# Kernel tuning notes

Hardware: AMD Instinct MI355X
Metric: run time of the kernel (lower is better)

Reference implementation:

```python
import jax, jax.numpy as jnp
import numpy as np

B, S, DM = 2, 2048, 1024
H, KH, HD = 16, 4, 64  # query heads, kv heads, head_dim
N_REP = H // KH


def rotate_half(u):
    d = u.shape[-1] // 2
    return jnp.concatenate([-u[..., d:], u[..., :d]], axis=-1)


def setup_inputs() -> dict:
    key = jax.random.key(0)
    ks = jax.random.split(key, 7)
    x = jax.random.normal(ks[0], (B, S, DM), dtype=jnp.float32)
    # RoPE tables (real rotary angles for realism)
    inv_freq = 1.0 / (10000.0 ** (jnp.arange(0, HD, 2, dtype=jnp.float32) / HD))
    t = jnp.arange(S, dtype=jnp.float32)
    freqs = jnp.outer(t, inv_freq)                      # [S, HD/2]
    emb = jnp.concatenate([freqs, freqs], axis=-1)      # [S, HD]
    cos, sin = jnp.cos(emb), jnp.sin(emb)
    sc = 0.02
    wq = jax.random.normal(ks[1], (DM, H * HD), dtype=jnp.float32) * sc
    wk = jax.random.normal(ks[2], (DM, KH * HD), dtype=jnp.float32) * sc
    wv = jax.random.normal(ks[3], (DM, KH * HD), dtype=jnp.float32) * sc
    wo = jax.random.normal(ks[4], (H * HD, DM), dtype=jnp.float32) * sc
    return {"x": x, "cos": cos, "sin": sin, "wq": wq, "wk": wk, "wv": wv, "wo": wo}


def reference(x, cos, sin, wq, wk, wv, wo):
    b, s, _ = x.shape
    # QKV projections (no bias)
    q = (x @ wq).reshape(b, s, H, HD)   # [b,s,H,HD]
    k = (x @ wk).reshape(b, s, KH, HD)  # [b,s,KH,HD]
    v = (x @ wv).reshape(b, s, KH, HD)
    # RoPE, broadcast cos/sin over the head axis
    c = cos[None, :s, None, :]
    sn = sin[None, :s, None, :]
    q = q * c + rotate_half(q) * sn
    k = k * c + rotate_half(k) * sn
    # GQA: repeat kv heads (repeat_interleave along head axis)
    k = jnp.repeat(k, N_REP, axis=2)  # [b,s,H,HD]
    v = jnp.repeat(v, N_REP, axis=2)
    # causal attention, full score matrix (non-flash path)
    scores = jnp.einsum("bqhd,bkhd->bhqk", q, k) / jnp.sqrt(jnp.float32(HD))
    causal = jnp.tril(jnp.ones((s, s), dtype=bool))
    scores = jnp.where(causal[None, None], scores, jnp.float32(-jnp.inf))
    attn = jax.nn.softmax(scores, axis=-1)
    out = jnp.einsum("bhqk,bkhd->bqhd", attn, v).reshape(b, s, H * HD)
    return out @ wo
```

## Files before the change

### kernel.cpp

```cpp
#include <hip/hip_runtime.h>
#include <hip/hip_bf16.h>

#define BATCH 2
#define SLEN  2048
#define DM    1024
#define NH    16
#define NKH   4
#define HD    64
#define NCH   4
#define PSTRIDE (BATCH * SLEN * NH * HD)
#define LSTRIDE (BATCH * SLEN * NH)

typedef __attribute__((ext_vector_type(8))) short short8;
typedef __attribute__((ext_vector_type(4))) float f32x4;

static __device__ __forceinline__ short f2bf(float x) {
    unsigned u = __float_as_uint(x);
    u += 0x7fffu + ((u >> 16) & 1u);
    return (short)(u >> 16);
}

static __device__ __forceinline__ void ldg_lds16(const short* g, short* l) {
    __builtin_amdgcn_global_load_lds(
        (const __attribute__((address_space(1))) unsigned int*)(const void*)g,
        (__attribute__((address_space(3))) unsigned int*)(void*)l,
        16, 0, 0);
}

#define QSCALE 0.1803368801f

__global__ __launch_bounds__(256) void prep_all(
    const float* __restrict__ wq, const float* __restrict__ wk,
    const float* __restrict__ wv, const float* __restrict__ wo,
    short* __restrict__ T,
    const float* __restrict__ X, short* __restrict__ Xb)
{
    const int by = blockIdx.y;
    const int t  = threadIdx.x;

    if (by >= 40) {
        const int blk = (by - 40) * 16 + blockIdx.x;
#pragma unroll
        for (int j = 0; j < 16; ++j) {
            const int i = blk * 4096 + j * 256 + t;
            const float4 v0 = ((const float4*)X)[i * 2];
            const float4 v1 = ((const float4*)X)[i * 2 + 1];
            __align__(16) short o[8];
            o[0] = f2bf(v0.x); o[1] = f2bf(v0.y); o[2] = f2bf(v0.z); o[3] = f2bf(v0.w);
            o[4] = f2bf(v1.x); o[5] = f2bf(v1.y); o[6] = f2bf(v1.z); o[7] = f2bf(v1.w);
            ((int4*)Xb)[i] = *(const int4*)o;
        }
        return;
    }

    const float* W; int Nc, rowoff, ntile;
    if (by < 16)      { W = wq; Nc = 1024; rowoff = 0;    ntile = by; }
    else if (by < 20) { W = wk; Nc = 256;  rowoff = 1024; ntile = by - 16; }
    else if (by < 24) { W = wv; Nc = 256;  rowoff = 1280; ntile = by - 20; }
    else              { W = wo; Nc = 1024; rowoff = 1536; ntile = by - 24; }
    const int kt = blockIdx.x * 64;
    const int nt = ntile * 64;
    __shared__ float tile[64][65];

#pragma unroll
    for (int i = 0; i < 4; ++i) {
        const int r = (t >> 4) + i * 16;
        const int c = (t & 15) * 4;
        const float4 v = *(const float4*)(W + (size_t)(kt + r) * Nc + nt + c);
        tile[r][c + 0] = v.x; tile[r][c + 1] = v.y;
        tile[r][c + 2] = v.z; tile[r][c + 3] = v.w;
    }
    __syncthreads();
#pragma unroll
    for (int i = 0; i < 2; ++i) {
        const int rr = (t >> 3) + i * 32;
        const int cc = (t & 7) * 8;
        __align__(16) short o[8];
#pragma unroll
        for (int j = 0; j < 8; ++j) o[j] = f2bf(tile[cc + j][rr]);
        *(int4*)(T + (size_t)(rowoff + nt + rr) * 1024 + kt + cc) = *(const int4*)o;
    }
}

template<int MODE>
__global__ __launch_bounds__(256) void gemm_abt(
    const short* __restrict__ A, const short* __restrict__ Bt,
    int M, int N, int K,
    float* __restrict__ Cf,
    short* __restrict__ Qb, short* __restrict__ Kb, short* __restrict__ Vb,
    const float* __restrict__ cosp, const float* __restrict__ sinp)
{
    const int t    = threadIdx.x;
    const int lane = t & 63;
    const int w    = t >> 6;
    const int l15  = lane & 15;
    const int l4   = lane >> 4;
    const int n0   = blockIdx.x * 128;
    const int m0   = blockIdx.y * 64;
    const int wm   = (w & 1) * 32;
    const int wn   = (w >> 1) * 64;

    __shared__ __align__(16) short As[64 * 64];
    __shared__ __align__(16) short Bs[128 * 64];

    f32x4 acc[2][4];
#pragma unroll
    for (int i = 0; i < 2; ++i)
#pragma unroll
        for (int j = 0; j < 4; ++j) acc[i][j] = (f32x4){0.f, 0.f, 0.f, 0.f};

    for (int kt = 0; kt < K; kt += 64) {
        __syncthreads();
#pragma unroll
        for (int i = 0; i < 2; ++i) {
            const int chunk = i * 256 + t;
            const int r = chunk >> 3;
            const int c = (chunk & 7) * 8;
            ldg_lds16(A + (size_t)(m0 + r) * K + kt + c, &As[chunk * 8]);
        }
#pragma unroll
        for (int i = 0; i < 4; ++i) {
            const int chunk = i * 256 + t;
            const int r = chunk >> 3;
            const int c = (chunk & 7) * 8;
            ldg_lds16(Bt + (size_t)(n0 + r) * K + kt + c, &Bs[chunk * 8]);
        }
        __syncthreads();

#pragma unroll
        for (int k2 = 0; k2 < 2; ++k2) {
            short8 af[2], bf[4];
#pragma unroll
            for (int i = 0; i < 2; ++i)
                af[i] = *(const short8*)&As[(wm + i * 16 + l15) * 64 + k2 * 32 + l4 * 8];
#pragma unroll
            for (int j = 0; j < 4; ++j)
                bf[j] = *(const short8*)&Bs[(wn + j * 16 + l15) * 64 + k2 * 32 + l4 * 8];
#pragma unroll
            for (int i = 0; i < 2; ++i)
#pragma unroll
                for (int j = 0; j < 4; ++j)
                    acc[i][j] = __builtin_amdgcn_mfma_f32_16x16x32_bf16(af[i], bf[j], acc[i][j], 0, 0, 0);
        }
    }

    if (MODE == 1) {
#pragma unroll
        for (int i = 0; i < 2; ++i)
#pragma unroll
            for (int j = 0; j < 4; ++j)
#pragma unroll
                for (int r = 0; r < 4; ++r) {
                    const int m = m0 + wm + i * 16 + l4 * 4 + r;
                    const int n = n0 + wn + j * 16 + l15;
                    Cf[(size_t)m * N + n] = acc[i][j][r];
                }
        return;
    }

    const int colbase = n0 + wn;
    if (colbase < 1024) {
        const int h = colbase >> 6;
#pragma unroll
        for (int i = 0; i < 2; ++i)
#pragma unroll
            for (int r = 0; r < 4; ++r) {
                const int m = m0 + wm + i * 16 + l4 * 4 + r;
                const int b = m >> 11, s = m & (SLEN - 1);
                short* dst = Qb + (((size_t)(b * SLEN + s) * NH + h) << 6);
#pragma unroll
                for (int j = 0; j < 2; ++j) {
                    const int d = j * 16 + l15;
                    const float cv = cosp[s * HD + d];
                    const float sv = sinp[s * HD + d];
                    const float a0 = acc[i][j][r];
                    const float a1 = acc[i][j + 2][r];
                    dst[d]      = f2bf((a0 * cv - a1 * sv) * QSCALE);
                    dst[d + 32] = f2bf((a1 * cv + a0 * sv) * QSCALE);
                }
            }
    } else if (colbase < 1280) {
        const int kh = (colbase - 1024) >> 6;
#pragma unroll
        for (int i = 0; i < 2; ++i)
#pragma unroll
            for (int r = 0; r < 4; ++r) {
                const int m = m0 + wm + i * 16 + l4 * 4 + r;
                const int b = m >> 11, s = m & (SLEN - 1);
                short* dst = Kb + (((size_t)(b * SLEN + s) * NKH + kh) << 6);
#pragma unroll
                for (int j = 0; j < 2; ++j) {
                    const int d = j * 16 + l15;
                    const float cv = cosp[s * HD + d];
                    const float sv = sinp[s * HD + d];
                    const float a0 = acc[i][j][r];
                    const float a1 = acc[i][j + 2][r];
                    dst[d]      = f2bf(a0 * cv - a1 * sv);
                    dst[d + 32] = f2bf(a1 * cv + a0 * sv);
                }
            }
    } else {
        const int kh = (colbase - 1280) >> 6;
#pragma unroll
        for (int i = 0; i < 2; ++i)
#pragma unroll
            for (int r = 0; r < 4; ++r) {
                const int m = m0 + wm + i * 16 + l4 * 4 + r;
                const int b = m >> 11, s = m & (SLEN - 1);
                short* dst = Vb + (((size_t)(b * SLEN + s) * NKH + kh) << 6);
#pragma unroll
                for (int j = 0; j < 4; ++j)
                    dst[j * 16 + l15] = f2bf(acc[i][j][r]);
            }
    }
}

__global__ __launch_bounds__(256) void vtrans_b(
    const short* __restrict__ Vb, short* __restrict__ Vt)
{
    const int s0 = blockIdx.x * 64;
    const int kh = blockIdx.y;
    const int b  = blockIdx.z;
    const int t  = threadIdx.x;
    __shared__ short tile[64][72];

#pragma unroll
    for (int i = 0; i < 2; ++i) {
        const int chunk = i * 256 + t;
        const int r = chunk >> 3;
        const int c = (chunk & 7) * 8;
        *(int4*)&tile[r][c] =
            *(const int4*)(Vb + (((size_t)(b * SLEN + s0 + r) * NKH + kh) << 6) + c);
    }
    __syncthreads();
#pragma unroll
    for (int i = 0; i < 2; ++i) {
        const int chunk = i * 256 + t;
        const int d  = chunk >> 3;
        const int sc = (chunk & 7) * 8;
        __align__(16) short o[8];
#pragma unroll
        for (int j = 0; j < 8; ++j) {
            const int sp = sc + j;
            const int u  = ((sp & 3) << 4) | (sp >> 2);
            o[j] = tile[u][d];
        }
        *(int4*)(Vt + ((size_t)((b * NKH + kh) * HD + d)) * SLEN + s0 + sc) = *(const int4*)o;
    }
}

__global__ __launch_bounds__(256, 4) void flash_mfma(
    const short* __restrict__ Qb,
    const short* __restrict__ Kb,
    const short* __restrict__ Vt,
    short* __restrict__ O,
    float* __restrict__ Op,
    float* __restrict__ Lp)
{
    const int qs = 63 - blockIdx.x;
    const int kc = blockIdx.y & 3;
    if (kc * 16 > qs) return;
    const int kh = blockIdx.y >> 2;
    const int b  = blockIdx.z;
    const int t    = threadIdx.x;
    const int lane = t & 63;
    const int w    = t >> 6;
    const int h    = kh * 4 + w;
    const int l15  = lane & 15;
    const int l4   = lane >> 4;
    const int q0   = qs * 32;
    const int sw   = l15 & 7;

    __shared__ __align__(16) short Ks[2][64 * 64];
    __shared__ __align__(16) short Vs[2][64 * 64];
    __shared__ __align__(16) short Ps[4][16 * 64];

    const int r_st  = t >> 3;
    const int c8_st = t & 7;

    short8 aq[2][2];
#pragma unroll
    for (int i = 0; i < 2; ++i)
#pragma unroll
        for (int ks = 0; ks < 2; ++ks)
            aq[i][ks] = *(const short8*)(
                Qb + ((size_t)((b * SLEN + q0 + i * 16 + l15) * NH + h)) * HD + ks * 32 + l4 * 8);

    f32x4 acc[2][4];
    f32x4 accl[2];
#pragma unroll
    for (int i = 0; i < 2; ++i) {
#pragma unroll
        for (int nt = 0; nt < 4; ++nt) acc[i][nt] = (f32x4){0.f, 0.f, 0.f, 0.f};
        accl[i] = (f32x4){0.f, 0.f, 0.f, 0.f};
    }

    const short8 ones8 = {0x3f80, 0x3f80, 0x3f80, 0x3f80, 0x3f80, 0x3f80, 0x3f80, 0x3f80};

    const int ntiles = (q0 >> 6) + 1;
    const int kt0  = kc * 8;
    const int kend = (kt0 + 8 < ntiles) ? kt0 + 8 : ntiles;

#define STAGE(BI, K0)                                                          \
    {                                                                          \
        _Pragma("unroll")                                                      \
        for (int i_ = 0; i_ < 2; ++i_) {                                       \
            const int r  = i_ * 32 + r_st;                                     \
            const int cs = (c8_st ^ (r & 7)) * 8;                              \
            const int ch = i_ * 256 + t;                                       \
            ldg_lds16(Kb + ((size_t)((b * SLEN + (K0) + r) * NKH + kh)) * HD + cs, \
                      &Ks[BI][ch * 8]);                                        \
            ldg_lds16(Vt + ((size_t)((b * NKH + kh) * HD + r)) * SLEN + (K0) + cs, \
                      &Vs[BI][ch * 8]);                                        \
        }                                                                      \
    }

    STAGE(0, kt0 * 64)

    for (int kt = kt0; kt < kend; ++kt) {
        const int bi = (kt - kt0) & 1;
        __syncthreads();
        if (kt + 1 < kend) STAGE(bi ^ 1, (kt + 1) * 64)

        f32x4 sf[2][4];
#pragma unroll
        for (int i = 0; i < 2; ++i)
#pragma unroll
            for (int f = 0; f < 4; ++f) sf[i][f] = (f32x4){0.f, 0.f, 0.f, 0.f};
#pragma unroll
        for (int ks = 0; ks < 2; ++ks)
#pragma unroll
            for (int f = 0; f < 4; ++f) {
                const short8 bk = *(const short8*)
                    &Ks[bi][(f * 16 + l15) * 64 + ((ks * 4 + l4) ^ sw) * 8];
#pragma unroll
                for (int i = 0; i < 2; ++i)
                    sf[i][f] = __builtin_amdgcn_mfma_f32_16x16x32_bf16(aq[i][ks], bk, sf[i][f], 0, 0, 0);
            }

        if (kt == ntiles - 1) {
            const int k0 = kt * 64;
#pragma unroll
            for (int i = 0; i < 2; ++i)
#pragma unroll
                for (int f = 0; f < 4; ++f)
#pragma unroll
                    for (int r = 0; r < 4; ++r)
                        if (k0 + f * 16 + l15 > q0 + i * 16 + l4 * 4 + r)
                            sf[i][f][r] = -1e30f;
        }

#pragma unroll
        for (int i = 0; i < 2; ++i) {
#pragma unroll
            for (int r = 0; r < 4; ++r) {
                __align__(8) short pk[4];
#pragma unroll
                for (int f = 0; f < 4; ++f) pk[f] = f2bf(exp2f(sf[i][f][r]));
                const int row = l4 * 4 + r;
                *(int2*)&Ps[w][row * 64 + (((l15 >> 1) ^ (row & 7)) << 3) + ((l15 & 1) << 2)] =
                    *(const int2*)pk;
            }
#pragma unroll
            for (int ks = 0; ks < 2; ++ks) {
                const short8 ap = *(const short8*)
                    &Ps[w][l15 * 64 + (((ks * 4 + l4) ^ (l15 & 7)) << 3)];
#pragma unroll
                for (int nt = 0; nt < 4; ++nt) {
                    const short8 bv = *(const short8*)
                        &Vs[bi][(nt * 16 + l15) * 64 + ((ks * 4 + l4) ^ sw) * 8];
                    acc[i][nt] = __builtin_amdgcn_mfma_f32_16x16x32_bf16(ap, bv, acc[i][nt], 0, 0, 0);
                }
                accl[i] = __builtin_amdgcn_mfma_f32_16x16x32_bf16(ap, ones8, accl[i], 0, 0, 0);
            }
        }
    }

    if (q0 < 512) {
#pragma unroll
        for (int i = 0; i < 2; ++i) {
            float rl[4];
#pragma unroll
            for (int r = 0; r < 4; ++r) rl[r] = 1.f / accl[i][r];
#pragma unroll
            for (int nt = 0; nt < 4; ++nt)
#pragma unroll
                for (int r = 0; r < 4; ++r) {
                    const int q = q0 + i * 16 + l4 * 4 + r;
                    O[((size_t)((b * SLEN + q) * NH + h)) * HD + nt * 16 + l15] =
                        f2bf(acc[i][nt][r] * rl[r]);
                }
        }
    } else {
        const size_t pbase = (size_t)kc * PSTRIDE;
#pragma unroll
        for (int i = 0; i < 2; ++i)
#pragma unroll
            for (int nt = 0; nt < 4; ++nt)
#pragma unroll
                for (int r = 0; r < 4; ++r) {
                    const int q = q0 + i * 16 + l4 * 4 + r;
                    Op[pbase + ((size_t)((b * SLEN + q) * NH + h)) * HD + nt * 16 + l15] =
                        acc[i][nt][r];
                }
        if (l15 == 0) {
#pragma unroll
            for (int i = 0; i < 2; ++i)
#pragma unroll
                for (int r = 0; r < 4; ++r) {
                    const int q = q0 + i * 16 + l4 * 4 + r;
                    Lp[(size_t)kc * LSTRIDE + (size_t)(b * SLEN + q) * NH + h] = accl[i][r];
                }
        }
    }
}

__global__ void combine_k(const float* __restrict__ Op, const float* __restrict__ Lp,
                          short* __restrict__ O)
{
    const int idx = blockIdx.x * 256 + threadIdx.x;
    const int dq = idx & 15;
    const int h  = (idx >> 4) & 15;
    const int rr = idx >> 8;
    const int b  = rr / 1536;
    const int s  = 512 + (rr - b * 1536);
    const int nact = (s >> 9) + 1;
    const size_t row = (size_t)(b * SLEN + s) * NH + h;

    float4 o = {0.f, 0.f, 0.f, 0.f};
    float l = 0.f;
    for (int kc = 0; kc < nact; ++kc) {
        const float4 p = *(const float4*)(Op + (size_t)kc * PSTRIDE + row * HD + dq * 4);
        o.x += p.x; o.y += p.y; o.z += p.z; o.w += p.w;
        l += Lp[(size_t)kc * LSTRIDE + row];
    }
    const float rl = 1.f / l;
    __align__(8) short pk[4];
    pk[0] = f2bf(o.x * rl); pk[1] = f2bf(o.y * rl);
    pk[2] = f2bf(o.z * rl); pk[3] = f2bf(o.w * rl);
    *(int2*)(O + row * HD + dq * 4) = *(const int2*)pk;
}

extern "C" void kernel_launch(void* const* d_in, const int* in_sizes, int n_in,
                              void* d_out, int out_size, void* d_ws, size_t ws_size,
                              hipStream_t stream) {
    const float* x    = (const float*)d_in[0];
    const float* cosp = (const float*)d_in[1];
    const float* sinp = (const float*)d_in[2];
    const float* wq   = (const float*)d_in[3];
    const float* wk   = (const float*)d_in[4];
    const float* wv   = (const float*)d_in[5];
    const float* wo   = (const float*)d_in[6];
    float* out = (float*)d_out;

    const int Mrows = BATCH * SLEN;

    short* xb = (short*)d_ws;
    short* Ob = xb;
    short* wT = xb + (size_t)Mrows * 1024;
    short* Qb = wT + (size_t)2560 * 1024;
    short* Kb = Qb + (size_t)Mrows * 1024;
    short* Vt = Kb + (size_t)Mrows * 256;
    short* Vb = Vt + (size_t)Mrows * 256;
    float* Op = (float*)(Vb + (size_t)Mrows * 256);
    float* Lp = Op + (size_t)NCH * PSTRIDE;

    prep_all<<<dim3(16, 48), 256, 0, stream>>>(wq, wk, wv, wo, wT, x, xb);

    gemm_abt<0><<<dim3(1536 / 128, Mrows / 64), 256, 0, stream>>>(
        xb, wT, Mrows, 1536, DM, nullptr, Qb, Kb, Vb, cosp, sinp);

    vtrans_b<<<dim3(SLEN / 64, NKH, BATCH), 256, 0, stream>>>(Vb, Vt);

    flash_mfma<<<dim3(SLEN / 32, NKH * NCH, BATCH), 256, 0, stream>>>(
        Qb, Kb, Vt, Ob, Op, Lp);

    combine_k<<<(BATCH * 1536 * NH * 16) / 256, 256, 0, stream>>>(Op, Lp, Ob);

    gemm_abt<1><<<dim3(DM / 128, Mrows / 64), 256, 0, stream>>>(
        Ob, wT + (size_t)1536 * 1024, Mrows, DM, DM, out,
        nullptr, nullptr, nullptr, nullptr, nullptr);
}
```

Before: 191.1 us.

## Register-prefetch double-buffered pipelines in GEMM and flash attention loops

The GEMM loop is converted from a single LDS buffer with two barriers per k-tile into a double-buffered scheme. The next tile is loaded into registers during compute and written to the alternate LDS buffer afterward, with an XOR swizzle added on the A/B tiles to reduce bank conflicts. The attention kernel replaces its async global-to-LDS staging with the same register prefetch. This aims to overlap global latency with MFMA work and remove one barrier per iteration, at the cost of extra VGPRs and doubled LDS in the GEMM, and __launch_bounds__(256,3) is added to keep occupancy.

```diff
diff --git a/kernel.cpp b/kernel.cpp
--- a/kernel.cpp
+++ b/kernel.cpp
@@ -83,7 +83,7 @@
 }
 
 template<int MODE>
-__global__ __launch_bounds__(256) void gemm_abt(
+__global__ __launch_bounds__(256, 3) void gemm_abt(
     const short* __restrict__ A, const short* __restrict__ Bt,
     int M, int N, int K,
     float* __restrict__ Cf,
@@ -100,8 +100,52 @@
     const int wm   = (w & 1) * 32;
     const int wn   = (w >> 1) * 64;
 
-    __shared__ __align__(16) short As[64 * 64];
-    __shared__ __align__(16) short Bs[128 * 64];
+    __shared__ __align__(16) short As[2][64 * 64];
+    __shared__ __align__(16) short Bs[2][128 * 64];
+
+    int4 areg[2], breg[4];
+
+#define G_GLL(BI, KT)                                                          \
+    {                                                                          \
+        _Pragma("unroll")                                                      \
+        for (int i_ = 0; i_ < 2; ++i_) {                                       \
+            const int ch = i_ * 256 + t;                                       \
+            const int r = ch >> 3, cs = ((ch & 7) ^ (r & 7)) * 8;              \
+            ldg_lds16(A + (size_t)(m0 + r) * K + (KT) + cs, &As[BI][ch * 8]);  \
+        }                                                                      \
+        _Pragma("unroll")                                                      \
+        for (int i_ = 0; i_ < 4; ++i_) {                                       \
+            const int ch = i_ * 256 + t;                                       \
+            const int r = ch >> 3, cs = ((ch & 7) ^ (r & 7)) * 8;              \
+            ldg_lds16(Bt + (size_t)(n0 + r) * K + (KT) + cs, &Bs[BI][ch * 8]); \
+        }                                                                      \
+    }
+
+#define G_LOADREG(KT)                                                          \
+    {                                                                          \
+        _Pragma("unroll")                                                      \
+        for (int i_ = 0; i_ < 2; ++i_) {                                       \
+            const int ch = i_ * 256 + t;                                       \
+            const int r = ch >> 3, cs = ((ch & 7) ^ (r & 7)) * 8;              \
+            areg[i_] = *(const int4*)(A + (size_t)(m0 + r) * K + (KT) + cs);   \
+        }                                                                      \
+        _Pragma("unroll")                                                      \
+        for (int i_ = 0; i_ < 4; ++i_) {                                       \
+            const int ch = i_ * 256 + t;                                       \
+            const int r = ch >> 3, cs = ((ch & 7) ^ (r & 7)) * 8;              \
+            breg[i_] = *(const int4*)(Bt + (size_t)(n0 + r) * K + (KT) + cs);  \
+        }                                                                      \
+    }
+
+#define G_WRITEREG(BI)                                                         \
+    {                                                                          \
+        _Pragma("unroll")                                                      \
+        for (int i_ = 0; i_ < 2; ++i_)                                         \
+            *(int4*)&As[BI][(i_ * 256 + t) * 8] = areg[i_];                    \
+        _Pragma("unroll")                                                      \
+        for (int i_ = 0; i_ < 4; ++i_)                                         \
+            *(int4*)&Bs[BI][(i_ * 256 + t) * 8] = breg[i_];                    \
+    }
 
     f32x4 acc[2][4];
 #pragma unroll
@@ -109,38 +153,33 @@
 #pragma unroll
         for (int j = 0; j < 4; ++j) acc[i][j] = (f32x4){0.f, 0.f, 0.f, 0.f};
 
+    G_GLL(0, 0)
+    G_LOADREG(64)
+
     for (int kt = 0; kt < K; kt += 64) {
+        const int bi = (kt >> 6) & 1;
         __syncthreads();
-#pragma unroll
-        for (int i = 0; i < 2; ++i) {
-            const int chunk = i * 256 + t;
-            const int r = chunk >> 3;
-            const int c = (chunk & 7) * 8;
-            ldg_lds16(A + (size_t)(m0 + r) * K + kt + c, &As[chunk * 8]);
-        }
-#pragma unroll
-        for (int i = 0; i < 4; ++i) {
-            const int chunk = i * 256 + t;
-            const int r = chunk >> 3;
-            const int c = (chunk & 7) * 8;
-            ldg_lds16(Bt + (size_t)(n0 + r) * K + kt + c, &Bs[chunk * 8]);
-        }
-        __syncthreads();
 
 #pragma unroll
         for (int k2 = 0; k2 < 2; ++k2) {
-            short8 af[2], bf[4];
+            const int pc = (((k2 * 4 + l4) ^ (l15 & 7)) << 3);
+            short8 af[2], bfr[4];
 #pragma unroll
             for (int i = 0; i < 2; ++i)
-                af[i] = *(const short8*)&As[(wm + i * 16 + l15) * 64 + k2 * 32 + l4 * 8];
+                af[i] = *(const short8*)&As[bi][(wm + i * 16 + l15) * 64 + pc];
 #pragma unroll
             for (int j = 0; j < 4; ++j)
-                bf[j] = *(const short8*)&Bs[(wn + j * 16 + l15) * 64 + k2 * 32 + l4 * 8];
+                bfr[j] = *(const short8*)&Bs[bi][(wn + j * 16 + l15) * 64 + pc];
 #pragma unroll
             for (int i = 0; i < 2; ++i)
 #pragma unroll
                 for (int j = 0; j < 4; ++j)
-                    acc[i][j] = __builtin_amdgcn_mfma_f32_16x16x32_bf16(af[i], bf[j], acc[i][j], 0, 0, 0);
+                    acc[i][j] = __builtin_amdgcn_mfma_f32_16x16x32_bf16(af[i], bfr[j], acc[i][j], 0, 0, 0);
+        }
+
+        if (kt + 64 < K) {
+            G_WRITEREG(bi ^ 1)
+            if (kt + 128 < K) G_LOADREG(kt + 128)
         }
     }
 
@@ -213,6 +252,9 @@
                     dst[j * 16 + l15] = f2bf(acc[i][j][r]);
             }
     }
+#undef G_GLL
+#undef G_LOADREG
+#undef G_WRITEREG
 }
 
 __global__ __launch_bounds__(256) void vtrans_b(
@@ -278,30 +320,9 @@
     const int r_st  = t >> 3;
     const int c8_st = t & 7;
 
-    short8 aq[2][2];
-#pragma unroll
-    for (int i = 0; i < 2; ++i)
-#pragma unroll
-        for (int ks = 0; ks < 2; ++ks)
-            aq[i][ks] = *(const short8*)(
-                Qb + ((size_t)((b * SLEN + q0 + i * 16 + l15) * NH + h)) * HD + ks * 32 + l4 * 8);
-
-    f32x4 acc[2][4];
-    f32x4 accl[2];
-#pragma unroll
-    for (int i = 0; i < 2; ++i) {
-#pragma unroll
-        for (int nt = 0; nt < 4; ++nt) acc[i][nt] = (f32x4){0.f, 0.f, 0.f, 0.f};
-        accl[i] = (f32x4){0.f, 0.f, 0.f, 0.f};
-    }
-
-    const short8 ones8 = {0x3f80, 0x3f80, 0x3f80, 0x3f80, 0x3f80, 0x3f80, 0x3f80, 0x3f80};
-
-    const int ntiles = (q0 >> 6) + 1;
-    const int kt0  = kc * 8;
-    const int kend = (kt0 + 8 < ntiles) ? kt0 + 8 : ntiles;
-
-#define STAGE(BI, K0)                                                          \
+    int4 kreg[2], vreg[2];
+
+#define F_GLL(BI, K0)                                                          \
     {                                                                          \
         _Pragma("unroll")                                                      \
         for (int i_ = 0; i_ < 2; ++i_) {                                       \
@@ -315,12 +336,56 @@
         }                                                                      \
     }
 
-    STAGE(0, kt0 * 64)
+#define F_LOADREG(K0)                                                          \
+    {                                                                          \
+        _Pragma("unroll")                                                      \
+        for (int i_ = 0; i_ < 2; ++i_) {                                       \
+            const int r  = i_ * 32 + r_st;                                     \
+            const int cs = (c8_st ^ (r & 7)) * 8;                              \
+            kreg[i_] = *(const int4*)(Kb + ((size_t)((b * SLEN + (K0) + r) * NKH + kh)) * HD + cs); \
+            vreg[i_] = *(const int4*)(Vt + ((size_t)((b * NKH + kh) * HD + r)) * SLEN + (K0) + cs); \
+        }                                                                      \
+    }
+
+#define F_WRITEREG(BI)                                                         \
+    {                                                                          \
+        _Pragma("unroll")                                                      \
+        for (int i_ = 0; i_ < 2; ++i_) {                                       \
+            const int ch = i_ * 256 + t;                                       \
+            *(int4*)&Ks[BI][ch * 8] = kreg[i_];                                \
+            *(int4*)&Vs[BI][ch * 8] = vreg[i_];                                \
+        }                                                                      \
+    }
+
+    short8 aq[2][2];
+#pragma unroll
+    for (int i = 0; i < 2; ++i)
+#pragma unroll
+        for (int ks = 0; ks < 2; ++ks)
+            aq[i][ks] = *(const short8*)(
+                Qb + ((size_t)((b * SLEN + q0 + i * 16 + l15) * NH + h)) * HD + ks * 32 + l4 * 8);
+
+    f32x4 acc[2][4];
+    f32x4 accl[2];
+#pragma unroll
+    for (int i = 0; i < 2; ++i) {
+#pragma unroll
+        for (int nt = 0; nt < 4; ++nt) acc[i][nt] = (f32x4){0.f, 0.f, 0.f, 0.f};
+        accl[i] = (f32x4){0.f, 0.f, 0.f, 0.f};
+    }
+
+    const short8 ones8 = {0x3f80, 0x3f80, 0x3f80, 0x3f80, 0x3f80, 0x3f80, 0x3f80, 0x3f80};
+
+    const int ntiles = (q0 >> 6) + 1;
+    const int kt0  = kc * 8;
+    const int kend = (kt0 + 8 < ntiles) ? kt0 + 8 : ntiles;
+
+    F_GLL(0, kt0 * 64)
+    if (kt0 + 1 < kend) F_LOADREG((kt0 + 1) * 64)
 
     for (int kt = kt0; kt < kend; ++kt) {
         const int bi = (kt - kt0) & 1;
         __syncthreads();
-        if (kt + 1 < kend) STAGE(bi ^ 1, (kt + 1) * 64)
 
         f32x4 sf[2][4];
 #pragma unroll
@@ -374,6 +439,11 @@
                 accl[i] = __builtin_amdgcn_mfma_f32_16x16x32_bf16(ap, ones8, accl[i], 0, 0, 0);
             }
         }
+
+        if (kt + 1 < kend) {
+            F_WRITEREG(bi ^ 1)
+            if (kt + 2 < kend) F_LOADREG((kt + 2) * 64)
+        }
     }
 
     if (q0 < 512) {
@@ -413,6 +483,9 @@
                 }
         }
     }
+#undef F_GLL
+#undef F_LOADREG
+#undef F_WRITEREG
 }
 
 __global__ void combine_k(const float* __restrict__ Op, const float* __restrict__ Lp,
```

Result: slower. 297.2 us (+55.5%).

## Swizzle GEMM LDS tiles and process KV in 128-key pairs without double buffering

Applied to the files above, without the earlier changes.

The GEMM kernel now applies an XOR swizzle to its A and B LDS tiles, both when staging and when reading fragments, to avoid LDS bank conflicts. The attention kernel drops its two-tile double-buffered K/V staging. It now loads 128 keys (a pair of 64-key tiles) per sync round into single larger buffers, halving the number of barriers. The cost is that global loads no longer overlap compute. Pairs that run past the causal end rely on the widened mask (kt >= ntiles-1) to zero out the extra tile, which still does the work of loading and computing that extra tile.

```diff
diff --git a/kernel.cpp b/kernel.cpp
--- a/kernel.cpp
+++ b/kernel.cpp
@@ -113,34 +113,33 @@
         __syncthreads();
 #pragma unroll
         for (int i = 0; i < 2; ++i) {
-            const int chunk = i * 256 + t;
-            const int r = chunk >> 3;
-            const int c = (chunk & 7) * 8;
-            ldg_lds16(A + (size_t)(m0 + r) * K + kt + c, &As[chunk * 8]);
+            const int ch = i * 256 + t;
+            const int r = ch >> 3, cs = ((ch & 7) ^ (r & 7)) * 8;
+            ldg_lds16(A + (size_t)(m0 + r) * K + kt + cs, &As[ch * 8]);
         }
 #pragma unroll
         for (int i = 0; i < 4; ++i) {
-            const int chunk = i * 256 + t;
-            const int r = chunk >> 3;
-            const int c = (chunk & 7) * 8;
-            ldg_lds16(Bt + (size_t)(n0 + r) * K + kt + c, &Bs[chunk * 8]);
+            const int ch = i * 256 + t;
+            const int r = ch >> 3, cs = ((ch & 7) ^ (r & 7)) * 8;
+            ldg_lds16(Bt + (size_t)(n0 + r) * K + kt + cs, &Bs[ch * 8]);
         }
         __syncthreads();
 
 #pragma unroll
         for (int k2 = 0; k2 < 2; ++k2) {
-            short8 af[2], bf[4];
+            const int pc = (((k2 * 4 + l4) ^ (l15 & 7)) << 3);
+            short8 af[2], bfr[4];
 #pragma unroll
             for (int i = 0; i < 2; ++i)
-                af[i] = *(const short8*)&As[(wm + i * 16 + l15) * 64 + k2 * 32 + l4 * 8];
+                af[i] = *(const short8*)&As[(wm + i * 16 + l15) * 64 + pc];
 #pragma unroll
             for (int j = 0; j < 4; ++j)
-                bf[j] = *(const short8*)&Bs[(wn + j * 16 + l15) * 64 + k2 * 32 + l4 * 8];
+                bfr[j] = *(const short8*)&Bs[(wn + j * 16 + l15) * 64 + pc];
 #pragma unroll
             for (int i = 0; i < 2; ++i)
 #pragma unroll
                 for (int j = 0; j < 4; ++j)
-                    acc[i][j] = __builtin_amdgcn_mfma_f32_16x16x32_bf16(af[i], bf[j], acc[i][j], 0, 0, 0);
+                    acc[i][j] = __builtin_amdgcn_mfma_f32_16x16x32_bf16(af[i], bfr[j], acc[i][j], 0, 0, 0);
         }
     }
 
@@ -271,12 +270,9 @@
     const int q0   = qs * 32;
     const int sw   = l15 & 7;
 
-    __shared__ __align__(16) short Ks[2][64 * 64];
-    __shared__ __align__(16) short Vs[2][64 * 64];
+    __shared__ __align__(16) short Ks[128 * 64];
+    __shared__ __align__(16) short Vs[64 * 128];
     __shared__ __align__(16) short Ps[4][16 * 64];
-
-    const int r_st  = t >> 3;
-    const int c8_st = t & 7;
 
     short8 aq[2][2];
 #pragma unroll
@@ -298,80 +294,85 @@
     const short8 ones8 = {0x3f80, 0x3f80, 0x3f80, 0x3f80, 0x3f80, 0x3f80, 0x3f80, 0x3f80};
 
     const int ntiles = (q0 >> 6) + 1;
-    const int kt0  = kc * 8;
-    const int kend = (kt0 + 8 < ntiles) ? kt0 + 8 : ntiles;
-
-#define STAGE(BI, K0)                                                          \
-    {                                                                          \
-        _Pragma("unroll")                                                      \
-        for (int i_ = 0; i_ < 2; ++i_) {                                       \
-            const int r  = i_ * 32 + r_st;                                     \
-            const int cs = (c8_st ^ (r & 7)) * 8;                              \
-            const int ch = i_ * 256 + t;                                       \
-            ldg_lds16(Kb + ((size_t)((b * SLEN + (K0) + r) * NKH + kh)) * HD + cs, \
-                      &Ks[BI][ch * 8]);                                        \
-            ldg_lds16(Vt + ((size_t)((b * NKH + kh) * HD + r)) * SLEN + (K0) + cs, \
-                      &Vs[BI][ch * 8]);                                        \
-        }                                                                      \
-    }
-
-    STAGE(0, kt0 * 64)
-
-    for (int kt = kt0; kt < kend; ++kt) {
-        const int bi = (kt - kt0) & 1;
+    const int kt0    = kc * 8;
+    const int kend   = (kt0 + 8 < ntiles) ? kt0 + 8 : ntiles;
+    const int npairs = (kend - kt0 + 1) >> 1;
+
+    for (int p = 0; p < npairs; ++p) {
+        const int tbase = kt0 + 2 * p;
+        const int k0p   = tbase * 64;
         __syncthreads();
-        if (kt + 1 < kend) STAGE(bi ^ 1, (kt + 1) * 64)
-
-        f32x4 sf[2][4];
-#pragma unroll
-        for (int i = 0; i < 2; ++i)
-#pragma unroll
-            for (int f = 0; f < 4; ++f) sf[i][f] = (f32x4){0.f, 0.f, 0.f, 0.f};
-#pragma unroll
-        for (int ks = 0; ks < 2; ++ks)
-#pragma unroll
-            for (int f = 0; f < 4; ++f) {
-                const short8 bk = *(const short8*)
-                    &Ks[bi][(f * 16 + l15) * 64 + ((ks * 4 + l4) ^ sw) * 8];
+#pragma unroll
+        for (int i = 0; i < 4; ++i) {
+            const int ch = i * 256 + t;
+            const int r = ch >> 3, cs = ((ch & 7) ^ (r & 7)) * 8;
+            ldg_lds16(Kb + ((size_t)((b * SLEN + k0p + r) * NKH + kh)) * HD + cs,
+                      &Ks[ch * 8]);
+        }
+#pragma unroll
+        for (int i = 0; i < 4; ++i) {
+            const int ch = i * 256 + t;
+            const int d = ch >> 4, cs = ((ch & 15) ^ (d & 15)) * 8;
+            ldg_lds16(Vt + ((size_t)((b * NKH + kh) * HD + d)) * SLEN + k0p + cs,
+                      &Vs[ch * 8]);
+        }
+        __syncthreads();
+
+#pragma unroll
+        for (int half = 0; half < 2; ++half) {
+            const int kt = tbase + half;
+
+            f32x4 sf[2][4];
+#pragma unroll
+            for (int i = 0; i < 2; ++i)
+#pragma unroll
+                for (int f = 0; f < 4; ++f) sf[i][f] = (f32x4){0.f, 0.f, 0.f, 0.f};
+#pragma unroll
+            for (int ks = 0; ks < 2; ++ks)
+#pragma unroll
+                for (int f = 0; f < 4; ++f) {
+                    const short8 bk = *(const short8*)
+                        &Ks[(half * 64 + f * 16 + l15) * 64 + ((ks * 4 + l4) ^ sw) * 8];
+#pragma unroll
+                    for (int i = 0; i < 2; ++i)
+                        sf[i][f] = __builtin_amdgcn_mfma_f32_16x16x32_bf16(aq[i][ks], bk, sf[i][f], 0, 0, 0);
+                }
+
+            if (kt >= ntiles - 1) {
+                const int k0 = kt * 64;
 #pragma unroll
                 for (int i = 0; i < 2; ++i)
-                    sf[i][f] = __builtin_amdgcn_mfma_f32_16x16x32_bf16(aq[i][ks], bk, sf[i][f], 0, 0, 0);
+#pragma unroll
+                    for (int f = 0; f < 4; ++f)
+#pragma unroll
+                        for (int r = 0; r < 4; ++r)
+                            if (k0 + f * 16 + l15 > q0 + i * 16 + l4 * 4 + r)
+                                sf[i][f][r] = -1e30f;
             }
 
-        if (kt == ntiles - 1) {
-            const int k0 = kt * 64;
-#pragma unroll
-            for (int i = 0; i < 2; ++i)
-#pragma unroll
-                for (int f = 0; f < 4; ++f)
-#pragma unroll
-                    for (int r = 0; r < 4; ++r)
-                        if (k0 + f * 16 + l15 > q0 + i * 16 + l4 * 4 + r)
-                            sf[i][f][r] = -1e30f;
-        }
-
-#pragma unroll
-        for (int i = 0; i < 2; ++i) {
-#pragma unroll
-            for (int r = 0; r < 4; ++r) {
-                __align__(8) short pk[4];
-#pragma unroll
-                for (int f = 0; f < 4; ++f) pk[f] = f2bf(exp2f(sf[i][f][r]));
-                const int row = l4 * 4 + r;
-                *(int2*)&Ps[w][row * 64 + (((l15 >> 1) ^ (row & 7)) << 3) + ((l15 & 1) << 2)] =
-                    *(const int2*)pk;
-            }
-#pragma unroll
-            for (int ks = 0; ks < 2; ++ks) {
-                const short8 ap = *(const short8*)
-                    &Ps[w][l15 * 64 + (((ks * 4 + l4) ^ (l15 & 7)) << 3)];
-#pragma unroll
-                for (int nt = 0; nt < 4; ++nt) {
-                    const short8 bv = *(const short8*)
-                        &Vs[bi][(nt * 16 + l15) * 64 + ((ks * 4 + l4) ^ sw) * 8];
-                    acc[i][nt] = __builtin_amdgcn_mfma_f32_16x16x32_bf16(ap, bv, acc[i][nt], 0, 0, 0);
-                }
-                accl[i] = __builtin_amdgcn_mfma_f32_16x16x32_bf16(ap, ones8, accl[i], 0, 0, 0);
+#pragma unroll
+            for (int i = 0; i < 2; ++i) {
+#pragma unroll
+                for (int r = 0; r < 4; ++r) {
+                    __align__(8) short pk[4];
+#pragma unroll
+                    for (int f = 0; f < 4; ++f) pk[f] = f2bf(exp2f(sf[i][f][r]));
+                    const int row = l4 * 4 + r;
+                    *(int2*)&Ps[w][row * 64 + (((l15 >> 1) ^ (row & 7)) << 3) + ((l15 & 1) << 2)] =
+                        *(const int2*)pk;
+                }
+#pragma unroll
+                for (int ks = 0; ks < 2; ++ks) {
+                    const short8 ap = *(const short8*)
+                        &Ps[w][l15 * 64 + (((ks * 4 + l4) ^ (l15 & 7)) << 3)];
+#pragma unroll
+                    for (int nt = 0; nt < 4; ++nt) {
+                        const short8 bv = *(const short8*)
+                            &Vs[(nt * 16 + l15) * 128 + (((half * 8 + ks * 4 + l4) ^ l15)) * 8];
+                        acc[i][nt] = __builtin_amdgcn_mfma_f32_16x16x32_bf16(ap, bv, acc[i][nt], 0, 0, 0);
+                    }
+                    accl[i] = __builtin_amdgcn_mfma_f32_16x16x32_bf16(ap, ones8, accl[i], 0, 0, 0);
+                }
             }
         }
     }
```

Result: slower. 208.7 us (+9.2%).
